# Performance work log

Measured on AMD Instinct MI355X. Metric: run time of the kernel, lower is better.

Reference implementation:

```python
import jax, jax.numpy as jnp
import numpy as np

N_EMBD = 1024
N_HEAD = 16
HEAD_SIZE = 64


def setup_inputs() -> dict:
    key = jax.random.key(0)
    ks = jax.random.split(key, 6)
    B, T, C, H, D = 2, 2048, N_EMBD, N_HEAD, HEAD_SIZE
    s = 1.0 / np.sqrt(C)
    x = jax.random.normal(ks[0], (B, T, C), dtype=jnp.float32)
    Wq = jax.random.normal(ks[1], (H, C, D), dtype=jnp.float32) * s
    Wk = jax.random.normal(ks[2], (H, C, D), dtype=jnp.float32) * s
    Wv = jax.random.normal(ks[3], (H, C, D), dtype=jnp.float32) * s
    Wo = jax.random.normal(ks[4], (H * D, C), dtype=jnp.float32) * (1.0 / np.sqrt(H * D))
    bo = jax.random.normal(ks[5], (C,), dtype=jnp.float32) * 0.01
    return {"x": x, "Wq": Wq, "Wk": Wk, "Wv": Wv, "Wo": Wo, "bo": bo}


def reference(x, Wq, Wk, Wv, Wo, bo):
    B, T, C = x.shape
    H, _, D = Wq.shape
    # Per-head projections, batched across heads: [B,H,T,D]
    q = jnp.einsum('btc,hcd->bhtd', x, Wq)
    k = jnp.einsum('btc,hcd->bhtd', x, Wk)
    v = jnp.einsum('btc,hcd->bhtd', x, Wv)
    # NOTE: original scales by sqrt(C) = sqrt(n_embd), not sqrt(head_size)
    scale = 1.0 / jnp.sqrt(jnp.float32(C))
    att = jnp.einsum('bhtd,bhsd->bhts', q, k) * scale  # [B,H,T,T]
    causal = jnp.tril(jnp.ones((T, T), dtype=bool))
    att = jnp.where(causal, att, -jnp.inf)
    att = jax.nn.softmax(att, axis=-1)
    # dropout omitted (eval mode / deterministic reference)
    out = jnp.einsum('bhts,bhsd->bhtd', att, v)  # [B,H,T,D]
    out = out.transpose(0, 2, 1, 3).reshape(B, T, H * D)
    return out @ Wo + bo
```

## Files before the change

### kernel.cpp

```cpp
#include <hip/hip_runtime.h>
#include <hip/hip_bf16.h>


typedef __hip_bfloat16 bf16;
typedef __bf16 v8bf __attribute__((ext_vector_type(8)));
typedef float  v4f  __attribute__((ext_vector_type(4)));
typedef unsigned long long u64;
typedef unsigned int u32;

#define MFMA16(a, b, c) __builtin_amdgcn_mfma_f32_16x16x32_bf16((a), (b), (c), 0, 0, 0)

__device__ __forceinline__ bf16 f2b(float x) { return __float2bfloat16(x); }
__device__ __forceinline__ __bf16 f2braw(float x) {
  bf16 t = __float2bfloat16(x);
  return *reinterpret_cast<__bf16*>(&t);
}
__device__ __forceinline__ unsigned short f2bu(float x) {
  bf16 t = __float2bfloat16(x);
  return *reinterpret_cast<unsigned short*>(&t);
}

__device__ __forceinline__ void load16_lds(const bf16* gptr, const bf16* lptr) {
  __builtin_amdgcn_global_load_lds(
      (const __attribute__((address_space(1))) u32*)gptr,
      (__attribute__((address_space(3))) u32*)lptr, 16, 0, 0);
}

__global__ __launch_bounds__(256) void prep_kernel(
    const float* __restrict__ x,
    const float* __restrict__ Wq, const float* __restrict__ Wk,
    const float* __restrict__ Wv, const float* __restrict__ Wo,
    bf16* __restrict__ xb, bf16* __restrict__ wt, bf16* __restrict__ wot)
{
  __shared__ float Lt[32][33];
  const int bid = blockIdx.x, tid = threadIdx.x;

  if (bid < 2048) {
    size_t i = ((size_t)bid * 256 + tid) * 8;
    float4 f0 = *(const float4*)(x + i);
    float4 f1 = *(const float4*)(x + i + 4);
    v8bf v;
    v[0] = f2braw(f0.x); v[1] = f2braw(f0.y); v[2] = f2braw(f0.z); v[3] = f2braw(f0.w);
    v[4] = f2braw(f1.x); v[5] = f2braw(f1.y); v[6] = f2braw(f1.z); v[7] = f2braw(f1.w);
    *(v8bf*)(xb + i) = v;
    return;
  }
  const int tx = tid & 31, ty = tid >> 5;
  if (bid < 5120) {
    const int idx = bid - 2048;
    const int z = idx >> 6, rem = idx & 63;
    const int p = z >> 4, h = z & 15;
    const float* ib = ((p == 0) ? Wq : (p == 1) ? Wk : Wv) + (size_t)h * 65536;
    bf16* ob = wt + (size_t)z * 65536;
    const int j0 = (rem & 1) * 32, i0 = (rem >> 1) * 32;
    #pragma unroll
    for (int r = 0; r < 4; ++r)
      Lt[ty + 8 * r][tx] = ib[(size_t)(i0 + ty + 8 * r) * 64 + j0 + tx];
    __syncthreads();
    #pragma unroll
    for (int r = 0; r < 4; ++r)
      ob[(size_t)(j0 + ty + 8 * r) * 1024 + i0 + tx] = f2b(Lt[tx][ty + 8 * r]);
  } else {
    const int idx = bid - 5120;
    const int j0 = (idx & 31) * 32, i0 = (idx >> 5) * 32;
    #pragma unroll
    for (int r = 0; r < 4; ++r)
      Lt[ty + 8 * r][tx] = Wo[(size_t)(i0 + ty + 8 * r) * 1024 + j0 + tx];
    __syncthreads();
    #pragma unroll
    for (int r = 0; r < 4; ++r)
      wot[(size_t)(j0 + ty + 8 * r) * 1024 + i0 + tx] = f2b(Lt[tx][ty + 8 * r]);
  }
}

__global__ __launch_bounds__(256) void qkv_gemm_kernel(
    const bf16* __restrict__ xb, const bf16* __restrict__ wt,
    bf16* __restrict__ qkv)
{
  __shared__ __align__(16) bf16 Ash[2][128][32];
  __shared__ __align__(16) bf16 Bsh[2][128][32];

  const int mt = blockIdx.x, nt = blockIdx.y;
  const int tid = threadIdx.x, w = tid >> 6, lane = tid & 63;
  const int ln = lane & 15, quad = lane >> 4;
  const int wm = w >> 1, wn = w & 1;
  const int m0 = mt * 128, n0 = nt * 128;

  const v4f vzero = {0.f, 0.f, 0.f, 0.f};
  v4f acc[4][4];
  #pragma unroll
  for (int mf = 0; mf < 4; ++mf)
    #pragma unroll
    for (int nf = 0; nf < 4; ++nf) acc[mf][nf] = vzero;

  const int srow = lane >> 2, sseg = (lane & 3) * 8;
  const bf16* ga = xb + (size_t)(m0 + 32 * w + srow) * 1024 + sseg;
  const bf16* gb = wt + (size_t)(n0 + 32 * w + srow) * 1024 + sseg;

  {
    load16_lds(ga,             &Ash[0][32 * w][0]);
    load16_lds(ga + 16 * 1024, &Ash[0][32 * w + 16][0]);
    load16_lds(gb,             &Bsh[0][32 * w][0]);
    load16_lds(gb + 16 * 1024, &Bsh[0][32 * w + 16][0]);
  }

  for (int kt = 0; kt < 32; ++kt) {
    const int buf = kt & 1;
    __syncthreads();

    v8bf af[4], bfv[4];
    #pragma unroll
    for (int mf = 0; mf < 4; ++mf)
      af[mf] = *(const v8bf*)&Ash[buf][wm * 64 + mf * 16 + ln][quad * 8];
    #pragma unroll
    for (int nf = 0; nf < 4; ++nf)
      bfv[nf] = *(const v8bf*)&Bsh[buf][wn * 64 + nf * 16 + ln][quad * 8];

    if (kt < 31) {
      const int k0 = (kt + 1) * 32, nb = buf ^ 1;
      load16_lds(ga + k0,             &Ash[nb][32 * w][0]);
      load16_lds(ga + 16 * 1024 + k0, &Ash[nb][32 * w + 16][0]);
      load16_lds(gb + k0,             &Bsh[nb][32 * w][0]);
      load16_lds(gb + 16 * 1024 + k0, &Bsh[nb][32 * w + 16][0]);
    }

    #pragma unroll
    for (int mf = 0; mf < 4; ++mf)
      #pragma unroll
      for (int nf = 0; nf < 4; ++nf)
        acc[mf][nf] = MFMA16(af[mf], bfv[nf], acc[mf][nf]);
  }

  const int jcol0 = n0 + wn * 64;
  const int p = jcol0 >> 10;
  const int h = (jcol0 >> 6) & 15;
  const float scale = (p == 0) ? 0.03125f : 1.0f;

  if (p < 2) {
    bf16* base = qkv + (size_t)p * 4194304 + (size_t)h * 262144;
    #pragma unroll
    for (int mf = 0; mf < 4; ++mf)
      #pragma unroll
      for (int nf = 0; nf < 4; ++nf) {
        int d = nf * 16 + ln;
        #pragma unroll
        for (int r = 0; r < 4; ++r) {
          int m = m0 + wm * 64 + mf * 16 + quad * 4 + r;
          base[(size_t)m * 64 + d] = f2b(acc[mf][nf][r] * scale);
        }
      }
  } else {
    bf16* vb = qkv + (size_t)2 * 4194304 + (size_t)h * 262144;
    #pragma unroll
    for (int mf = 0; mf < 4; ++mf) {
      int mrow = m0 + wm * 64 + mf * 16 + quad * 4;
      int bi = mrow >> 11, t0 = mrow & 2047;
      #pragma unroll
      for (int nf = 0; nf < 4; ++nf) {
        int d = nf * 16 + ln;
        u64 pk = (u64)f2bu(acc[mf][nf][0]) |
                 ((u64)f2bu(acc[mf][nf][1]) << 16) |
                 ((u64)f2bu(acc[mf][nf][2]) << 32) |
                 ((u64)f2bu(acc[mf][nf][3]) << 48);
        *(u64*)(vb + (size_t)bi * 131072 + (size_t)d * 2048 + t0) = pk;
      }
    }
  }
}

__global__ __launch_bounds__(128) void attn_kernel(
    const bf16* __restrict__ qkv, bf16* __restrict__ att)
{
  __shared__ __align__(16) bf16 Ksh[2][2][64][32];
  __shared__ __align__(16) bf16 Vsh[2][2][64][32];
  __shared__ __align__(16) __bf16 Psh[2][16][72];

  const int fid = blockIdx.x;
  const int mtraw = fid & 31;
  const int mt = ((fid >> 8) & 1) ? (31 - mtraw) : mtraw;
  const int grp = (fid >> 5) & 31;
  const int b = grp >> 4, h = grp & 15;
  const int row0 = mt * 64;

  const int tid = threadIdx.x, w = tid >> 6, lane = tid & 63;
  const int ln = lane & 15, quad = lane >> 4;

  const bf16* qbase  = qkv + (size_t)h * 262144 + (size_t)b * 131072;
  const bf16* kbase  = qbase + 4194304;
  const bf16* vtbase = qbase + 8388608;

  const int wrow = row0 + w * 32;
  v8bf aq[2][2];
  #pragma unroll
  for (int mc = 0; mc < 2; ++mc)
    #pragma unroll
    for (int ks = 0; ks < 2; ++ks)
      aq[mc][ks] = *(const v8bf*)(qbase +
          (size_t)(wrow + mc * 16 + ln) * 64 + ks * 32 + quad * 8);

  v8bf vone;
  {
    unsigned short u = 0x3F80;
    __bf16 one_e = *reinterpret_cast<__bf16*>(&u);
    #pragma unroll
    for (int j = 0; j < 8; ++j) vone[j] = one_e;
  }

  const v4f vzero = {0.f, 0.f, 0.f, 0.f};
  v4f o[2][4], lacc[2];
  #pragma unroll
  for (int mc = 0; mc < 2; ++mc) {
    lacc[mc] = vzero;
    #pragma unroll
    for (int n = 0; n < 4; ++n) o[mc][n] = vzero;
  }

  const float NEG = -30000.0f;
  const int kb_end = mt;
  const int srow = lane >> 2, sseg = (lane & 3) * 8;

  const bf16* gk0 = kbase + (size_t)(w * 32 + srow) * 64 + sseg;
  const bf16* gv0 = vtbase + (size_t)(w * 32 + srow) * 2048 + sseg;

  #define STAGE(KB, BUF)                                                     \
    {                                                                        \
      const bf16* gk = gk0 + (size_t)(KB) * 64 * 64;                         \
      load16_lds(gk,            &Ksh[BUF][0][w * 32][0]);                    \
      load16_lds(gk + 32,       &Ksh[BUF][1][w * 32][0]);                    \
      load16_lds(gk + 1024,     &Ksh[BUF][0][w * 32 + 16][0]);               \
      load16_lds(gk + 1056,     &Ksh[BUF][1][w * 32 + 16][0]);               \
      const bf16* gv = gv0 + (KB) * 64;                                      \
      load16_lds(gv,            &Vsh[BUF][0][w * 32][0]);                    \
      load16_lds(gv + 32,       &Vsh[BUF][1][w * 32][0]);                    \
      load16_lds(gv + 32768,    &Vsh[BUF][0][w * 32 + 16][0]);               \
      load16_lds(gv + 32800,    &Vsh[BUF][1][w * 32 + 16][0]);               \
    }

  STAGE(0, 0)

  for (int kb = 0; kb <= kb_end; ++kb) {
    const int buf = kb & 1;
    __syncthreads();

    v8bf kf[2][4], vf[2][4];
    #pragma unroll
    for (int nf = 0; nf < 4; ++nf) {
      kf[0][nf] = *(const v8bf*)&Ksh[buf][0][nf * 16 + ln][quad * 8];
      kf[1][nf] = *(const v8bf*)&Ksh[buf][1][nf * 16 + ln][quad * 8];
      vf[0][nf] = *(const v8bf*)&Vsh[buf][0][nf * 16 + ln][quad * 8];
      vf[1][nf] = *(const v8bf*)&Vsh[buf][1][nf * 16 + ln][quad * 8];
    }

    if (kb < kb_end) STAGE(kb + 1, buf ^ 1)

    #pragma unroll
    for (int mc = 0; mc < 2; ++mc) {
      v4f s[4];
      #pragma unroll
      for (int nf = 0; nf < 4; ++nf) s[nf] = vzero;
      #pragma unroll
      for (int ks = 0; ks < 2; ++ks)
        #pragma unroll
        for (int nf = 0; nf < 4; ++nf)
          s[nf] = MFMA16(aq[mc][ks], kf[ks][nf], s[nf]);

      if (kb == kb_end) {
        int row = wrow + mc * 16 + quad * 4;
        #pragma unroll
        for (int nf = 0; nf < 4; ++nf) {
          int col = kb * 64 + nf * 16 + ln;
          #pragma unroll
          for (int r = 0; r < 4; ++r)
            if (col > row + r) s[nf][r] = NEG;
        }
      }

      #pragma unroll
      for (int nf = 0; nf < 4; ++nf)
        #pragma unroll
        for (int r = 0; r < 4; ++r)
          Psh[w][quad * 4 + r][nf * 16 + ln] = f2braw(__expf(s[nf][r]));
      __asm__ volatile("s_waitcnt lgkmcnt(0)" ::: "memory");

      #pragma unroll
      for (int ks = 0; ks < 2; ++ks) {
        v8bf pf = *(const v8bf*)&Psh[w][ln][ks * 32 + quad * 8];
        lacc[mc] = MFMA16(pf, vone, lacc[mc]);
        #pragma unroll
        for (int nf = 0; nf < 4; ++nf)
          o[mc][nf] = MFMA16(pf, vf[ks][nf], o[mc][nf]);
      }
    }
  }
  #undef STAGE

  #pragma unroll
  for (int mc = 0; mc < 2; ++mc) {
    v4f inv;
    #pragma unroll
    for (int r = 0; r < 4; ++r) inv[r] = 1.0f / lacc[mc][r];
    #pragma unroll
    for (int nf = 0; nf < 4; ++nf)
      #pragma unroll
      for (int r = 0; r < 4; ++r) {
        int m = b * 2048 + wrow + mc * 16 + quad * 4 + r;
        att[(size_t)m * 1024 + h * 64 + nf * 16 + ln] = f2b(o[mc][nf][r] * inv[r]);
      }
  }
}

__global__ __launch_bounds__(256) void out_gemm_kernel(
    const bf16* __restrict__ att, const bf16* __restrict__ wot,
    const float* __restrict__ bo, float* __restrict__ out)
{
  __shared__ __align__(16) bf16 Ash[2][128][32];
  __shared__ __align__(16) bf16 Bsh[2][64][32];

  const int mt = blockIdx.x, nt = blockIdx.y;
  const int tid = threadIdx.x, w = tid >> 6, lane = tid & 63;
  const int ln = lane & 15, quad = lane >> 4;
  const int wm = w >> 1, wn = w & 1;
  const int m0 = mt * 128, n0 = nt * 64;

  const v4f vzero = {0.f, 0.f, 0.f, 0.f};
  v4f acc[4][2];
  #pragma unroll
  for (int mf = 0; mf < 4; ++mf)
    #pragma unroll
    for (int nf = 0; nf < 2; ++nf) acc[mf][nf] = vzero;

  const int srow = lane >> 2, sseg = (lane & 3) * 8;
  const bf16* ga = att + (size_t)(m0 + 32 * w + srow) * 1024 + sseg;
  const bf16* gb = wot + (size_t)(n0 + 16 * w + srow) * 1024 + sseg;

  {
    load16_lds(ga,             &Ash[0][32 * w][0]);
    load16_lds(ga + 16 * 1024, &Ash[0][32 * w + 16][0]);
    load16_lds(gb,             &Bsh[0][16 * w][0]);
  }

  for (int kt = 0; kt < 32; ++kt) {
    const int buf = kt & 1;
    __syncthreads();

    v8bf af[4], bfv[2];
    #pragma unroll
    for (int mf = 0; mf < 4; ++mf)
      af[mf] = *(const v8bf*)&Ash[buf][wm * 64 + mf * 16 + ln][quad * 8];
    #pragma unroll
    for (int nf = 0; nf < 2; ++nf)
      bfv[nf] = *(const v8bf*)&Bsh[buf][wn * 32 + nf * 16 + ln][quad * 8];

    if (kt < 31) {
      const int k0 = (kt + 1) * 32, nb = buf ^ 1;
      load16_lds(ga + k0,             &Ash[nb][32 * w][0]);
      load16_lds(ga + 16 * 1024 + k0, &Ash[nb][32 * w + 16][0]);
      load16_lds(gb + k0,             &Bsh[nb][16 * w][0]);
    }

    #pragma unroll
    for (int mf = 0; mf < 4; ++mf)
      #pragma unroll
      for (int nf = 0; nf < 2; ++nf)
        acc[mf][nf] = MFMA16(af[mf], bfv[nf], acc[mf][nf]);
  }

  #pragma unroll
  for (int nf = 0; nf < 2; ++nf) {
    int j = n0 + wn * 32 + nf * 16 + ln;
    float bias = bo[j];
    #pragma unroll
    for (int mf = 0; mf < 4; ++mf)
      #pragma unroll
      for (int r = 0; r < 4; ++r) {
        int m = m0 + wm * 64 + mf * 16 + quad * 4 + r;
        out[(size_t)m * 1024 + j] = acc[mf][nf][r] + bias;
      }
  }
}

extern "C" void kernel_launch(void* const* d_in, const int* in_sizes, int n_in,
                              void* d_out, int out_size, void* d_ws, size_t ws_size,
                              hipStream_t stream) {
  const float* x  = (const float*)d_in[0];
  const float* Wq = (const float*)d_in[1];
  const float* Wk = (const float*)d_in[2];
  const float* Wv = (const float*)d_in[3];
  const float* Wo = (const float*)d_in[4];
  const float* bo = (const float*)d_in[5];
  float* out = (float*)d_out;

  bf16* xb  = (bf16*)d_ws;
  bf16* wt  = xb + 4194304;
  bf16* wot = xb + 7340032;
  bf16* qkv = xb + 8388608;
  bf16* att = xb + 20971520;

  prep_kernel<<<6144, 256, 0, stream>>>(x, Wq, Wk, Wv, Wo, xb, wt, wot);
  qkv_gemm_kernel<<<dim3(32, 24), 256, 0, stream>>>(xb, wt, qkv);
  attn_kernel<<<1024, 128, 0, stream>>>(qkv, att);
  out_gemm_kernel<<<dim3(32, 16), 256, 0, stream>>>(att, wot, bo, out);
}
```

Baseline: 182.8 us.

## Restructure attention: transposed S so P stays in registers, swizzled LDS, paired tiles

The attention kernel now computes S transposed (K as the A operand), so the exp'd P fragment lands directly in the register layout needed for the PV MFMA. This removes the Psh shared-memory round trip and its wait. K/V tiles are stored in a 64-wide XOR-swizzled LDS layout with permuted K rows to avoid bank conflicts. Each 256-thread block (4 waves of 16 rows) processes a pair of causal tiles (mt and 31-mt) in sequence to balance work, and the grid is halved. The costs are an extra barrier between halves and reliance on the permuted-row mapping being correct.

```diff
diff --git a/kernel.cpp b/kernel.cpp
--- a/kernel.cpp
+++ b/kernel.cpp
@@ -168,19 +168,16 @@
   }
 }
 
-__global__ __launch_bounds__(128) void attn_kernel(
+__global__ __launch_bounds__(256, 2) void attn_kernel(
     const bf16* __restrict__ qkv, bf16* __restrict__ att)
 {
-  __shared__ __align__(16) bf16 Ksh[2][2][64][32];
-  __shared__ __align__(16) bf16 Vsh[2][2][64][32];
-  __shared__ __align__(16) __bf16 Psh[2][16][72];
+  __shared__ __align__(16) bf16 Ksh[2][64][64];
+  __shared__ __align__(16) bf16 Vsh[2][64][64];
 
   const int fid = blockIdx.x;
-  const int mtraw = fid & 31;
-  const int mt = ((fid >> 8) & 1) ? (31 - mtraw) : mtraw;
-  const int grp = (fid >> 5) & 31;
+  const int pairid = fid >> 5;
+  const int grp = fid & 31;
   const int b = grp >> 4, h = grp & 15;
-  const int row0 = mt * 64;
 
   const int tid = threadIdx.x, w = tid >> 6, lane = tid & 63;
   const int ln = lane & 15, quad = lane >> 4;
@@ -189,72 +186,75 @@
   const bf16* kbase  = qbase + 4194304;
   const bf16* vtbase = qbase + 8388608;
 
-  const int wrow = row0 + w * 32;
-  v8bf aq[2][2];
-  #pragma unroll
-  for (int mc = 0; mc < 2; ++mc)
-    #pragma unroll
-    for (int ks = 0; ks < 2; ++ks)
-      aq[mc][ks] = *(const v8bf*)(qbase +
-          (size_t)(wrow + mc * 16 + ln) * 64 + ks * 32 + quad * 8);
+  const int l8 = lane & 7, r8 = lane >> 3;
+  const int slot = l8 ^ r8;
+  const int p0 = w * 16 + r8, p1 = p0 + 8;
+  const int kp0 = (p0 & 32) | ((p0 & 12) << 1) | ((p0 & 16) >> 2) | (p0 & 3);
+  const int kp1 = (p1 & 32) | ((p1 & 12) << 1) | ((p1 & 16) >> 2) | (p1 & 3);
+  const bf16* gk0 = kbase + kp0 * 64 + slot * 8;
+  const bf16* gk1 = kbase + kp1 * 64 + slot * 8;
+  const bf16* gv0 = vtbase + (w * 16 + r8) * 2048 + slot * 8;
+  const bf16* gv1 = gv0 + 8 * 2048;
+
+  const int sw = ln & 7;
+  const int c0 = ((quad    ) ^ sw) * 8;
+  const int c1 = ((quad + 4) ^ sw) * 8;
+  const int rowoff = ln * 64;
 
   v8bf vone;
   {
     unsigned short u = 0x3F80;
-    __bf16 one_e = *reinterpret_cast<__bf16*>(&u);
-    #pragma unroll
-    for (int j = 0; j < 8; ++j) vone[j] = one_e;
-  }
-
+    __bf16 e = *reinterpret_cast<__bf16*>(&u);
+    #pragma unroll
+    for (int j = 0; j < 8; ++j) vone[j] = e;
+  }
   const v4f vzero = {0.f, 0.f, 0.f, 0.f};
-  v4f o[2][4], lacc[2];
-  #pragma unroll
-  for (int mc = 0; mc < 2; ++mc) {
-    lacc[mc] = vzero;
-    #pragma unroll
-    for (int n = 0; n < 4; ++n) o[mc][n] = vzero;
-  }
-
   const float NEG = -30000.0f;
-  const int kb_end = mt;
-  const int srow = lane >> 2, sseg = (lane & 3) * 8;
-
-  const bf16* gk0 = kbase + (size_t)(w * 32 + srow) * 64 + sseg;
-  const bf16* gv0 = vtbase + (size_t)(w * 32 + srow) * 2048 + sseg;
-
-  #define STAGE(KB, BUF)                                                     \
-    {                                                                        \
-      const bf16* gk = gk0 + (size_t)(KB) * 64 * 64;                         \
-      load16_lds(gk,            &Ksh[BUF][0][w * 32][0]);                    \
-      load16_lds(gk + 32,       &Ksh[BUF][1][w * 32][0]);                    \
-      load16_lds(gk + 1024,     &Ksh[BUF][0][w * 32 + 16][0]);               \
-      load16_lds(gk + 1056,     &Ksh[BUF][1][w * 32 + 16][0]);               \
-      const bf16* gv = gv0 + (KB) * 64;                                      \
-      load16_lds(gv,            &Vsh[BUF][0][w * 32][0]);                    \
-      load16_lds(gv + 32,       &Vsh[BUF][1][w * 32][0]);                    \
-      load16_lds(gv + 32768,    &Vsh[BUF][0][w * 32 + 16][0]);               \
-      load16_lds(gv + 32800,    &Vsh[BUF][1][w * 32 + 16][0]);               \
-    }
-
-  STAGE(0, 0)
-
-  for (int kb = 0; kb <= kb_end; ++kb) {
-    const int buf = kb & 1;
-    __syncthreads();
-
-    v8bf kf[2][4], vf[2][4];
-    #pragma unroll
-    for (int nf = 0; nf < 4; ++nf) {
-      kf[0][nf] = *(const v8bf*)&Ksh[buf][0][nf * 16 + ln][quad * 8];
-      kf[1][nf] = *(const v8bf*)&Ksh[buf][1][nf * 16 + ln][quad * 8];
-      vf[0][nf] = *(const v8bf*)&Vsh[buf][0][nf * 16 + ln][quad * 8];
-      vf[1][nf] = *(const v8bf*)&Vsh[buf][1][nf * 16 + ln][quad * 8];
-    }
-
-    if (kb < kb_end) STAGE(kb + 1, buf ^ 1)
-
-    #pragma unroll
-    for (int mc = 0; mc < 2; ++mc) {
+
+  #define STAGE(KB, BUF) {                                       \
+    load16_lds(gk0 + (KB) * 4096, &Ksh[BUF][w * 16][0]);         \
+    load16_lds(gk1 + (KB) * 4096, &Ksh[BUF][w * 16 + 8][0]);     \
+    load16_lds(gv0 + (KB) * 64,   &Vsh[BUF][w * 16][0]);         \
+    load16_lds(gv1 + (KB) * 64,   &Vsh[BUF][w * 16 + 8][0]); }
+
+  #pragma unroll 1
+  for (int half = 0; half < 2; ++half) {
+    const int mt = half ? (31 - pairid) : pairid;
+    const int row0 = mt * 64;
+    const int wrow = row0 + w * 16;
+    const int qg = wrow + ln;
+
+    v8bf aq[2];
+    #pragma unroll
+    for (int ks = 0; ks < 2; ++ks)
+      aq[ks] = *(const v8bf*)(qbase + (size_t)(wrow + ln) * 64 + ks * 32 + quad * 8);
+
+    v4f o[4], lacc;
+    lacc = vzero;
+    #pragma unroll
+    for (int dt = 0; dt < 4; ++dt) o[dt] = vzero;
+
+    if (half) __syncthreads();
+    STAGE(0, 0)
+
+    const int kb_end = mt;
+    for (int kb = 0; kb <= kb_end; ++kb) {
+      const int buf = kb & 1;
+      __syncthreads();
+
+      v8bf kf[2][4], vf[2][4];
+      const bf16* kr = &Ksh[buf][0][0];
+      const bf16* vr = &Vsh[buf][0][0];
+      #pragma unroll
+      for (int nf = 0; nf < 4; ++nf) {
+        kf[0][nf] = *(const v8bf*)(kr + nf * 1024 + rowoff + c0);
+        kf[1][nf] = *(const v8bf*)(kr + nf * 1024 + rowoff + c1);
+        vf[0][nf] = *(const v8bf*)(vr + nf * 1024 + rowoff + c0);
+        vf[1][nf] = *(const v8bf*)(vr + nf * 1024 + rowoff + c1);
+      }
+
+      if (kb < kb_end) STAGE(kb + 1, buf ^ 1)
+
       v4f s[4];
       #pragma unroll
       for (int nf = 0; nf < 4; ++nf) s[nf] = vzero;
@@ -262,51 +262,48 @@
       for (int ks = 0; ks < 2; ++ks)
         #pragma unroll
         for (int nf = 0; nf < 4; ++nf)
-          s[nf] = MFMA16(aq[mc][ks], kf[ks][nf], s[nf]);
+          s[nf] = MFMA16(kf[ks][nf], aq[ks], s[nf]);
 
       if (kb == kb_end) {
-        int row = wrow + mc * 16 + quad * 4;
         #pragma unroll
         for (int nf = 0; nf < 4; ++nf) {
-          int col = kb * 64 + nf * 16 + ln;
+          const int kc = kb * 64 + (nf >> 1) * 32 + quad * 8 + (nf & 1) * 4;
           #pragma unroll
           for (int r = 0; r < 4; ++r)
-            if (col > row + r) s[nf][r] = NEG;
+            if (kc + r > qg) s[nf][r] = NEG;
         }
       }
 
-      #pragma unroll
-      for (int nf = 0; nf < 4; ++nf)
+      v8bf pa[2];
+      #pragma unroll
+      for (int ks = 0; ks < 2; ++ks)
         #pragma unroll
-        for (int r = 0; r < 4; ++r)
-          Psh[w][quad * 4 + r][nf * 16 + ln] = f2braw(__expf(s[nf][r]));
-      __asm__ volatile("s_waitcnt lgkmcnt(0)" ::: "memory");
-
-      #pragma unroll
-      for (int ks = 0; ks < 2; ++ks) {
-        v8bf pf = *(const v8bf*)&Psh[w][ln][ks * 32 + quad * 8];
-        lacc[mc] = MFMA16(pf, vone, lacc[mc]);
+        for (int hh = 0; hh < 2; ++hh)
+          #pragma unroll
+          for (int r = 0; r < 4; ++r)
+            pa[ks][hh * 4 + r] = f2braw(__expf(s[2 * ks + hh][r]));
+
+      lacc = MFMA16(pa[0], vone, lacc);
+      lacc = MFMA16(pa[1], vone, lacc);
+      #pragma unroll
+      for (int ks = 0; ks < 2; ++ks)
         #pragma unroll
-        for (int nf = 0; nf < 4; ++nf)
-          o[mc][nf] = MFMA16(pf, vf[ks][nf], o[mc][nf]);
-      }
+        for (int dt = 0; dt < 4; ++dt)
+          o[dt] = MFMA16(pa[ks], vf[ks][dt], o[dt]);
     }
+
+    v4f inv;
+    #pragma unroll
+    for (int r = 0; r < 4; ++r) inv[r] = 1.0f / lacc[r];
+    #pragma unroll
+    for (int dt = 0; dt < 4; ++dt)
+      #pragma unroll
+      for (int r = 0; r < 4; ++r) {
+        int m = b * 2048 + wrow + quad * 4 + r;
+        att[(size_t)m * 1024 + h * 64 + dt * 16 + ln] = f2b(o[dt][r] * inv[r]);
+      }
   }
   #undef STAGE
-
-  #pragma unroll
-  for (int mc = 0; mc < 2; ++mc) {
-    v4f inv;
-    #pragma unroll
-    for (int r = 0; r < 4; ++r) inv[r] = 1.0f / lacc[mc][r];
-    #pragma unroll
-    for (int nf = 0; nf < 4; ++nf)
-      #pragma unroll
-      for (int r = 0; r < 4; ++r) {
-        int m = b * 2048 + wrow + mc * 16 + quad * 4 + r;
-        att[(size_t)m * 1024 + h * 64 + nf * 16 + ln] = f2b(o[mc][nf][r] * inv[r]);
-      }
-  }
 }
 
 __global__ __launch_bounds__(256) void out_gemm_kernel(
@@ -398,6 +395,6 @@
 
   prep_kernel<<<6144, 256, 0, stream>>>(x, Wq, Wk, Wv, Wo, xb, wt, wot);
   qkv_gemm_kernel<<<dim3(32, 24), 256, 0, stream>>>(xb, wt, qkv);
-  attn_kernel<<<1024, 128, 0, stream>>>(qkv, att);
+  attn_kernel<<<512, 256, 0, stream>>>(qkv, att);
   out_gemm_kernel<<<dim3(32, 16), 256, 0, stream>>>(att, wot, bo, out);
 }
```

After: 165.7 us. 9.4% less time.
